# Kernel tuning notes

Measured on AMD Instinct MI355X. Metric: run time of the kernel, lower is better.

Reference implementation:

```python
import jax, jax.numpy as jnp
import numpy as np

B, N, C, H, W = 8, 512, 3, 16, 16
K, P, E = 2, 4, 1           # K: hop levels == filter taps, P: attn heads, E: edge feature sets
SLOPE = 0.2                 # LeakyReLU slope in attention
GAT_DIMS = {'d0': (128, 128), 'd1': (512, 32), 'u0': (128, 64),
            'u1': (256, 128), 's0': (128, 128), 's1': (512, 64)}


def _conv(x, w, b):
    pad = w.shape[-1] // 2
    y = jax.lax.conv_general_dilated(x, w, (1, 1), [(pad, pad), (pad, pad)],
                                     dimension_numbers=('NCHW', 'OIHW', 'NCHW'))
    return y + b[None, :, None, None]


def _gat(x, S, wk, wq, wf, b):
    # x: (B,G,N); S: (B,E,N,N) binary GSO. KeyQuery attention + K-tap attentional filter.
    key = jnp.einsum('pegf,bgn->bpefn', wk, x)
    qry = jnp.einsum('pegf,bgn->bpefn', wq, x)
    # scores[...,n,m]: logit of node n attending to neighbor m
    scores = jax.nn.leaky_relu(jnp.einsum('bpefn,bpefm->bpenm', qry, key), SLOPE)
    mask = (jnp.abs(S) > 1e-9)[:, None]                    # (B,1,E,N,N)
    aij = jnp.where(mask, jax.nn.softmax(jnp.where(mask, scores, -1e9), axis=-1), 0.0)
    Pn, En, Kt, G, F = wf.shape
    xk = jnp.broadcast_to(x[:, None, None], (x.shape[0], Pn, En, G, x.shape[-1]))
    zs = [xk]
    for _ in range(Kt - 1):
        xk = jnp.einsum('bpegm,bpenm->bpegn', xk, aij)     # attention-weighted diffusion
        zs.append(xk)
    z = jnp.stack(zs, axis=3)                              # (B,P,E,K,G,N)
    y = jnp.einsum('bpekgn,pekgf->bpfn', z, wf) + b[None, None, :, None]
    y = jax.nn.relu(y)                                     # nonlinearity before head concat
    return y.reshape(y.shape[0], Pn * F, y.shape[-1])      # (B, P*F, N)


def _forward(x, Slist, conv0_w, conv0_b, conv1_w, conv1_b, flat_w, flat_b,
             d0_wk, d0_wq, d0_wf, d0_b, d1_wk, d1_wq, d1_wf, d1_b,
             u0_wk, u0_wq, u0_wf, u0_b, u1_wk, u1_wq, u1_wf, u1_b,
             s0_wk, s0_wq, s0_wf, s0_b, s1_wk, s1_wq, s1_wf, s1_b,
             dec0_w, dec0_b, dec1_w, dec1_b):
    Bn, Nn = x.shape[0], x.shape[1]
    h = x.reshape(Bn * Nn, C, H, W)
    e = jax.nn.relu(_conv(h, conv0_w, conv0_b))
    e = jax.nn.relu(_conv(e, conv1_w, conv1_b))
    e = e + h                                              # RES connection after encoder
    f = jax.nn.relu(e.reshape(Bn * Nn, -1) @ flat_w.T + flat_b)
    g = f.reshape(Bn, -1, Nn)                              # faithful torch reshape to (B, F, N)
    S0, S1 = Slist[:, 0:1], Slist[:, 1:2]
    p0 = g
    p1 = _gat(p0, S0, d0_wk, d0_wq, d0_wf, d0_b)           # downward pass
    p2 = _gat(p1, S1, d1_wk, d1_wq, d1_wf, d1_b)
    # upward pass + shortcuts (upward[l] uses S[K-l-1]; shortcut[K-1-l] on p[K-1-l])
    u0 = _gat(p2, S1, u0_wk, u0_wq, u0_wf, u0_b) + _gat(p1, S1, s1_wk, s1_wq, s1_wf, s1_b)
    u1 = _gat(u0, S0, u1_wk, u1_wq, u1_wf, u1_b) + _gat(p0, S0, s0_wk, s0_wq, s0_wf, s0_b)
    d = jax.nn.relu(u1.reshape(Bn * Nn, -1) @ dec0_w.T + dec0_b)
    out = jax.nn.softmax(d @ dec1_w.T + dec1_b, axis=-1)   # nn.Softmax() -> dim=1 on 2D input
    return out.reshape(Bn, Nn, -1)


def setup_inputs() -> dict:
    key = jax.random.key(0)
    ks = iter(jax.random.split(key, 64))
    def nrm(shape, s=0.1):
        return jax.random.normal(next(ks), shape, jnp.float32) * s
    x = jax.random.normal(next(ks), (B, N, C, H, W), jnp.float32)
    adj = (jax.random.uniform(next(ks), (B, K, N, N)) < 0.02).astype(jnp.float32)
    Slist = jnp.clip(adj + jnp.eye(N, dtype=jnp.float32)[None, None], 0.0, 1.0)
    inp = {'x': x, 'Slist': Slist,
           'conv0_w': nrm((32, C, 3, 3)), 'conv0_b': nrm((32,)),
           'conv1_w': nrm((C, 32, 3, 3)), 'conv1_b': nrm((C,)),
           'flat_w': nrm((128, C * H * W)), 'flat_b': nrm((128,))}
    for pre, (G, F) in GAT_DIMS.items():
        inp[pre + '_wk'] = nrm((P, E, G, F))
        inp[pre + '_wq'] = nrm((P, E, G, F))
        inp[pre + '_wf'] = nrm((P, E, K, G, F))
        inp[pre + '_b'] = nrm((F,))
    inp.update({'dec0_w': nrm((256, 512)), 'dec0_b': nrm((256,)),
                'dec1_w': nrm((5, 256)), 'dec1_b': nrm((5,))})
    return inp


def reference(x, Slist, conv0_w, conv0_b, conv1_w, conv1_b, flat_w, flat_b,
              d0_wk, d0_wq, d0_wf, d0_b, d1_wk, d1_wq, d1_wf, d1_b,
              u0_wk, u0_wq, u0_wf, u0_b, u1_wk, u1_wq, u1_wf, u1_b,
              s0_wk, s0_wq, s0_wf, s0_b, s1_wk, s1_wq, s1_wf, s1_b,
              dec0_w, dec0_b, dec1_w, dec1_b):
    return _forward(x, Slist, conv0_w, conv0_b, conv1_w, conv1_b, flat_w, flat_b,
                    d0_wk, d0_wq, d0_wf, d0_b, d1_wk, d1_wq, d1_wf, d1_b,
                    u0_wk, u0_wq, u0_wf, u0_b, u1_wk, u1_wq, u1_wf, u1_b,
                    s0_wk, s0_wq, s0_wf, s0_b, s1_wk, s1_wq, s1_wf, s1_b,
                    dec0_w, dec0_b, dec1_w, dec1_b)
```

## Files before the change

kernel.cpp:

```cpp
#include <hip/hip_runtime.h>
#include <hip/hip_bf16.h>
#include <math.h>

typedef unsigned short u16;
typedef unsigned int   u32;
typedef unsigned long long u64;

#define CAP 48

__device__ __forceinline__ float tof(u16 u){
  union { u32 i; float f; } v; v.i = ((u32)u) << 16; return v.f;
}
__device__ __forceinline__ u16 fromf(float f){
  union { float f; u32 i; } v; v.f = f;
  u32 x = v.i;
  return (u16)((x + 0x7fffu + ((x >> 16) & 1u)) >> 16);
}

__global__ void detect_dtype(const void* xp, int* flag){
  if(threadIdx.x == 0 && blockIdx.x == 0){
    const u16* p = (const u16*)xp;
    int outl = 0;
    for(int i = 0; i < 128; i++){
      u16 u = p[2*i];
      int e = (u >> 7) & 0xFF;
      if(u != 0 && (e < 100 || e > 140)) outl++;
    }
    *flag = (outl > 32) ? 1 : 0;
  }
}

struct WArgs {
  const void* p[34];
  int sz[34];
  int off[35];
};

__global__ __launch_bounds__(256) void convert_weights(WArgs wa, const int* flag,
                                                       float* __restrict__ arena, int total){
  int i = blockIdx.x * 256 + threadIdx.x;
  if(i >= total) return;
  int isf = *flag;
  int t = 0;
  while(wa.off[t+1] <= i) t++;
  int j = i - wa.off[t];
  float v = 0.f;
  if(j < wa.sz[t])
    v = isf ? ((const float*)wa.p[t])[j] : tof(((const u16*)wa.p[t])[j]);
  arena[i] = v;
}

__global__ __launch_bounds__(256) void transpose_w(const float* __restrict__ src,
                                                   float* __restrict__ dst, int R, int C){
  int i = blockIdx.x * 256 + threadIdx.x;
  if(i < R*C){
    int r = i / C, c = i - r*C;
    dst[(size_t)c*R + r] = src[i];
  }
}

__global__ __launch_bounds__(64) void build_nbr(const void* __restrict__ S,
                                                int* __restrict__ nbr_idx,
                                                int* __restrict__ nbr_cnt,
                                                const int* __restrict__ flag){
  int isf = *flag;
  int row  = blockIdx.x;
  int lane = threadIdx.x;
  int cnt = 0;
  for(int c = 0; c < 8; c++){
    int m = c*64 + lane;
    size_t idx = (size_t)row * 512 + m;
    float sv = isf ? ((const float*)S)[idx] : tof(((const u16*)S)[idx]);
    bool pred = fabsf(sv) > 1e-9f;
    unsigned long long mask = __ballot(pred);
    int pos = cnt + __popcll(mask & ((1ull << lane) - 1ull));
    if(pred && pos < CAP) nbr_idx[(size_t)row*CAP + pos] = m;
    cnt += __popcll(mask);
  }
  if(lane == 0) nbr_cnt[row] = cnt > CAP ? CAP : cnt;
}

__global__ __launch_bounds__(256) void encoder_conv(
    const void* __restrict__ x, const int* __restrict__ flag,
    const float* __restrict__ w0, const float* __restrict__ b0,
    const float* __restrict__ w1, const float* __restrict__ b1,
    float* __restrict__ e1n)
{
  __shared__ float xpad[3][18][18];
  __shared__ float e0p[16][18][18];

  int isf = *flag;
  int tid = threadIdx.x;
  size_t img = blockIdx.x;
  int py = tid >> 4, px = tid & 15;

  float* z1 = &xpad[0][0][0];
  for(int i = tid; i < 972; i += 256) z1[i] = 0.f;
  float* z2 = &e0p[0][0][0];
  for(int i = tid; i < 5184; i += 256) z2[i] = 0.f;
  __syncthreads();

  #pragma unroll
  for(int i = 0; i < 3; i++){
    size_t gi = img*768 + i*256 + tid;
    xpad[i][1+py][1+px] = isf ? ((const float*)x)[gi] : tof(((const u16*)x)[gi]);
  }
  __syncthreads();

  float acc1[3] = {0.f, 0.f, 0.f};

  for(int grp = 0; grp < 2; grp++){
    float acc0[16];
    #pragma unroll
    for(int o = 0; o < 16; o++) acc0[o] = 0.f;
    for(int i = 0; i < 3; i++){
      float rr[9];
      #pragma unroll
      for(int ky = 0; ky < 3; ky++)
        #pragma unroll
        for(int kx = 0; kx < 3; kx++)
          rr[ky*3+kx] = xpad[i][py+ky][px+kx];
      #pragma unroll
      for(int o = 0; o < 16; o++){
        #pragma unroll
        for(int t = 0; t < 9; t++)
          acc0[o] = fmaf(rr[t], w0[(grp*16+o)*27 + i*9 + t], acc0[o]);
      }
    }
    __syncthreads();
    #pragma unroll
    for(int o = 0; o < 16; o++)
      e0p[o][1+py][1+px] = fmaxf(acc0[o] + b0[grp*16 + o], 0.f);
    __syncthreads();

    for(int i = 0; i < 16; i++){
      float rr[9];
      #pragma unroll
      for(int ky = 0; ky < 3; ky++)
        #pragma unroll
        for(int kx = 0; kx < 3; kx++)
          rr[ky*3+kx] = e0p[i][py+ky][px+kx];
      int ic = grp*16 + i;
      #pragma unroll
      for(int o = 0; o < 3; o++){
        #pragma unroll
        for(int t = 0; t < 9; t++)
          acc1[o] = fmaf(rr[t], w1[o*288 + ic*9 + t], acc1[o]);
      }
    }
  }

  #pragma unroll
  for(int o = 0; o < 3; o++)
    e1n[img*768 + o*256 + tid] = fmaxf(acc1[o] + b1[o], 0.f) + xpad[o][1+py][1+px];
}

__global__ __launch_bounds__(256) void gemm_flat(
    const float* __restrict__ e1n, const float* __restrict__ fwT,
    const float* __restrict__ fb, float* __restrict__ g)
{
  __shared__ float As[16][68];
  __shared__ float Bs[16][68];
  int tid = threadIdx.x;
  int n0 = blockIdx.x * 64, m0 = blockIdx.y * 64;

  int lk = tid >> 4;
  int l4 = (tid & 15) * 4;
  int br = tid >> 2;
  int bc = (tid & 3) * 4;

  float acc[4][4];
  #pragma unroll
  for(int i = 0; i < 4; i++)
    #pragma unroll
    for(int jj = 0; jj < 4; jj++) acc[i][jj] = 0.f;

  int tm = tid >> 4, tn = tid & 15;
  for(int kt = 0; kt < 48; kt++){
    int k0 = kt*16;
    *(float4*)&As[lk][l4] = *(const float4*)&fwT[(size_t)(k0 + lk)*128 + m0 + l4];
    float4 bv = *(const float4*)&e1n[(size_t)(n0 + br)*768 + k0 + bc];
    Bs[bc+0][br] = bv.x; Bs[bc+1][br] = bv.y; Bs[bc+2][br] = bv.z; Bs[bc+3][br] = bv.w;
    __syncthreads();
    #pragma unroll
    for(int kk = 0; kk < 16; kk++){
      float4 a  = *(const float4*)&As[kk][tm*4];
      float4 xx = *(const float4*)&Bs[kk][tn*4];
      float av[4]  = {a.x, a.y, a.z, a.w};
      float xvv[4] = {xx.x, xx.y, xx.z, xx.w};
      #pragma unroll
      for(int i = 0; i < 4; i++)
        #pragma unroll
        for(int jj = 0; jj < 4; jj++)
          acc[i][jj] = fmaf(av[i], xvv[jj], acc[i][jj]);
    }
    __syncthreads();
  }

  #pragma unroll
  for(int jj = 0; jj < 4; jj++){
    int img = n0 + tn*4 + jj;
    float4 r = make_float4(fmaxf(acc[0][jj] + fb[m0+tm*4+0], 0.f),
                           fmaxf(acc[1][jj] + fb[m0+tm*4+1], 0.f),
                           fmaxf(acc[2][jj] + fb[m0+tm*4+2], 0.f),
                           fmaxf(acc[3][jj] + fb[m0+tm*4+3], 0.f));
    *(float4*)&g[(size_t)img*128 + m0 + tm*4] = r;
  }
}

struct KqP { const float* X; const float* wk; const float* wq; float* kqT;
             int G, F, my; };

__global__ __launch_bounds__(256) void gemm_kq2(KqP A, KqP B)
{
  __shared__ float Ws[32*68];
  __shared__ float Xs[32*68];
  int tid = threadIdx.x;
  int by = blockIdx.y;
  KqP P = (by < A.my) ? A : B;
  int lby = (by < A.my) ? by : (by - A.my);
  int bp = blockIdx.z;
  int b = bp >> 2, p = bp & 3;
  int n0 = blockIdx.x * 64, m0 = lby * 64;
  const float* Xb = P.X + (size_t)b * P.G * 512;

  int lk = tid >> 4;
  int l4 = (tid & 15) * 4;

  int mg = m0 + l4;
  int quad = mg / P.F;
  int mq = mg - quad * P.F;
  size_t GF = (size_t)P.G * P.F;
  const float* wb = (quad == 0 ? P.wk : P.wq) + (size_t)p * GF + mq;

  float acc[4][4];
  #pragma unroll
  for(int i = 0; i < 4; i++)
    #pragma unroll
    for(int jj = 0; jj < 4; jj++) acc[i][jj] = 0.f;

  int tm = tid >> 4, tn = tid & 15;
  int KT = P.G / 32;
  for(int kt = 0; kt < KT; kt++){
    int k = kt*32 + lk;
    *(float4*)&Ws[lk*68 + l4]      = *(const float4*)(wb + (size_t)k * P.F);
    *(float4*)&Ws[(lk+16)*68 + l4] = *(const float4*)(wb + (size_t)(k+16) * P.F);
    *(float4*)&Xs[lk*68 + l4]      = *(const float4*)(Xb + (size_t)k * 512 + n0 + l4);
    *(float4*)&Xs[(lk+16)*68 + l4] = *(const float4*)(Xb + (size_t)(k+16) * 512 + n0 + l4);
    __syncthreads();
    #pragma unroll
    for(int kk = 0; kk < 32; kk++){
      float4 a  = *(const float4*)&Ws[kk*68 + tm*4];
      float4 xx = *(const float4*)&Xs[kk*68 + tn*4];
      float av[4]  = {a.x, a.y, a.z, a.w};
      float xvv[4] = {xx.x, xx.y, xx.z, xx.w};
      #pragma unroll
      for(int i = 0; i < 4; i++)
        #pragma unroll
        for(int jj = 0; jj < 4; jj++)
          acc[i][jj] = fmaf(av[i], xvv[jj], acc[i][jj]);
    }
    __syncthreads();
  }

  int F2 = 2*P.F;
  float* ob = P.kqT + (size_t)bp * 512 * F2;
  #pragma unroll
  for(int jj = 0; jj < 4; jj++){
    float* orow = ob + (size_t)(n0 + tn*4 + jj) * F2 + m0 + tm*4;
    #pragma unroll
    for(int i = 0; i < 4; i++) orow[i] = acc[i][jj];
  }
}

__global__ __launch_bounds__(256) void gemm_kqK64(
    const float* __restrict__ X,
    const float* __restrict__ wk, const float* __restrict__ wq,
    float* __restrict__ kqT, int G, int F)
{
  __shared__ float Ws[64][68];
  __shared__ float Xs[64][68];
  int tid = threadIdx.x;
  int bp = blockIdx.z;
  int b = bp >> 2, p = bp & 3;
  int n0 = blockIdx.x * 64, m0 = blockIdx.y * 64;
  const float* Xb = X + (size_t)b * G * 512;

  int lk = tid >> 4;
  int l4 = (tid & 15) * 4;

  int mg = m0 + l4;
  int quad = mg / F;
  int mq = mg - quad * F;
  size_t GF = (size_t)G * F;
  const float* wb = (quad == 0 ? wk : wq) + (size_t)p * GF + mq;

  float acc[4][4];
  #pragma unroll
  for(int i = 0; i < 4; i++)
    #pragma unroll
    for(int jj = 0; jj < 4; jj++) acc[i][jj] = 0.f;

  int tm = tid >> 4, tn = tid & 15;
  int KT = G / 64;
  for(int kt = 0; kt < KT; kt++){
    #pragma unroll
    for(int kb = 0; kb < 4; kb++){
      int k = kt*64 + lk + kb*16;
      *(float4*)&Ws[lk + kb*16][l4] = *(const float4*)(wb + (size_t)k * F);
      *(float4*)&Xs[lk + kb*16][l4] = *(const float4*)(Xb + (size_t)k * 512 + n0 + l4);
    }
    __syncthreads();
    #pragma unroll
    for(int kk = 0; kk < 64; kk++){
      float4 a  = *(const float4*)&Ws[kk][tm*4];
      float4 xx = *(const float4*)&Xs[kk][tn*4];
      float av[4]  = {a.x, a.y, a.z, a.w};
      float xvv[4] = {xx.x, xx.y, xx.z, xx.w};
      #pragma unroll
      for(int i = 0; i < 4; i++)
        #pragma unroll
        for(int jj = 0; jj < 4; jj++)
          acc[i][jj] = fmaf(av[i], xvv[jj], acc[i][jj]);
    }
    __syncthreads();
  }

  int F2 = 2*F;
  float* ob = kqT + (size_t)bp * 512 * F2;
  #pragma unroll
  for(int jj = 0; jj < 4; jj++){
    float* orow = ob + (size_t)(n0 + tn*4 + jj) * F2 + m0 + tm*4;
    #pragma unroll
    for(int i = 0; i < 4; i++) orow[i] = acc[i][jj];
  }
}

struct AtP { const float* kqT; u64* ctrl; int F, s; };

__global__ __launch_bounds__(256) void attn2(
    AtP A, AtP B,
    const int* __restrict__ nbr_idx, const int* __restrict__ nbr_cnt)
{
  __shared__ float qs[16][132];
  __shared__ float sc[16][CAP];
  __shared__ float red[16][2];
  int tid = threadIdx.x;
  int n0 = blockIdx.x * 16;
  int bp = blockIdx.y;
  AtP P = (blockIdx.z == 0) ? A : B;
  int b = bp >> 2;
  int F = P.F;
  int F2 = 2*F;
  const float* kqT = P.kqT;

  int F4 = F >> 2;
  for(int i = tid; i < 16*F4; i += 256){
    int r = i / F4, c4 = (i - r*F4) * 4;
    *(float4*)&qs[r][c4] =
      *(const float4*)&kqT[((size_t)bp*512 + n0 + r)*F2 + F + c4];
  }
  __syncthreads();

  int r = tid >> 4;
  int t = tid & 15;
  int n = n0 + r;
  int srow = (b*2 + P.s)*512 + n;
  int cnt = nbr_cnt[srow];
  const int* il = nbr_idx + (size_t)srow * CAP;

  for(int j = t; j < cnt; j += 16){
    int m = il[j];
    const float* krow = kqT + ((size_t)bp*512 + m)*F2;
    float a = 0.f;
    for(int f = 0; f < F; f += 4){
      float4 k4 = *(const float4*)&krow[f];
      a = fmaf(qs[r][f],   k4.x, a);
      a = fmaf(qs[r][f+1], k4.y, a);
      a = fmaf(qs[r][f+2], k4.z, a);
      a = fmaf(qs[r][f+3], k4.w, a);
    }
    sc[r][j] = a >= 0.f ? a : 0.2f * a;
  }
  __syncthreads();

  if(t == 0){
    float mx = -1e30f;
    for(int j = 0; j < cnt; j++) mx = fmaxf(mx, sc[r][j]);
    float ssum = 0.f;
    for(int j = 0; j < cnt; j++) ssum += expf(sc[r][j] - mx);
    red[r][0] = mx; red[r][1] = ssum;
  }
  __syncthreads();

  float mx = red[r][0], ssum = red[r][1];
  u64* crow = P.ctrl + ((size_t)bp*512 + n)*CAP;
  for(int j = t; j < cnt; j += 16){
    float w = expf(sc[r][j] - mx) / ssum;
    crow[j] = (u64)__float_as_uint(w) | ((u64)(u32)il[j] << 32);
  }
}

struct FiP { const float* X; const u64* ctrl; float* Xp; int G, s, gy; };

__global__ __launch_bounds__(256) void fill_Xp4(
    FiP A, FiP B, const int* __restrict__ nbr_cnt)
{
  __shared__ float xi[512*18];

  int tid = threadIdx.x;
  int by = blockIdx.y;
  FiP P = (by < A.gy) ? A : B;
  int lby = (by < A.gy) ? by : (by - A.gy);
  int n0 = blockIdx.x * 64;
  int g0 = lby * 16;
  int bp = blockIdx.z;
  int b = bp >> 2;
  int srow0 = (b*2 + P.s)*512 + n0;

  const float* Xb = P.X + ((size_t)b * P.G + g0) * 512;
  for(int i = tid; i < 16*512; i += 256){
    int gl = i >> 9, m = i & 511;
    xi[m*18 + gl] = Xb[(size_t)gl*512 + m];
  }

  int n_l = tid & 63;
  int q   = tid >> 6;
  int cnt = nbr_cnt[srow0 + n_l];
  const u64* cn = P.ctrl + ((size_t)bp*512 + n0 + n_l)*CAP;
  __syncthreads();

  const float* xq = &xi[4*q];
  float a0=0.f, a1=0.f, a2=0.f, a3=0.f;
  for(int j0 = 0; j0 < cnt; j0 += 4){
    u64 c0 = cn[j0], c1 = cn[j0+1], c2 = cn[j0+2], c3 = cn[j0+3];
    int m0 = (int)(c0 >> 32) & 511;
    int m1 = (int)(c1 >> 32) & 511;
    int m2 = (int)(c2 >> 32) & 511;
    int m3 = (int)(c3 >> 32) & 511;
    float w0 = __uint_as_float((u32)c0);
    float w1 = (j0+1 < cnt) ? __uint_as_float((u32)c1) : 0.f;
    float w2 = (j0+2 < cnt) ? __uint_as_float((u32)c2) : 0.f;
    float w3 = (j0+3 < cnt) ? __uint_as_float((u32)c3) : 0.f;
    float2 g0a = *(const float2*)&xq[m0*18], g0b = *(const float2*)&xq[m0*18 + 2];
    float2 g1a = *(const float2*)&xq[m1*18], g1b = *(const float2*)&xq[m1*18 + 2];
    float2 g2a = *(const float2*)&xq[m2*18], g2b = *(const float2*)&xq[m2*18 + 2];
    float2 g3a = *(const float2*)&xq[m3*18], g3b = *(const float2*)&xq[m3*18 + 2];
    a0 = fmaf(w0, g0a.x, a0); a1 = fmaf(w0, g0a.y, a1);
    a2 = fmaf(w0, g0b.x, a2); a3 = fmaf(w0, g0b.y, a3);
    a0 = fmaf(w1, g1a.x, a0); a1 = fmaf(w1, g1a.y, a1);
    a2 = fmaf(w1, g1b.x, a2); a3 = fmaf(w1, g1b.y, a3);
    a0 = fmaf(w2, g2a.x, a0); a1 = fmaf(w2, g2a.y, a1);
    a2 = fmaf(w2, g2b.x, a2); a3 = fmaf(w2, g2b.y, a3);
    a0 = fmaf(w3, g3a.x, a0); a1 = fmaf(w3, g3a.y, a1);
    a2 = fmaf(w3, g3b.x, a2); a3 = fmaf(w3, g3b.y, a3);
  }

  float* ob = P.Xp + ((size_t)bp * P.G + g0 + 4*q) * 512 + n0 + n_l;
  ob[0]    = a0;
  ob[512]  = a1;
  ob[1024] = a2;
  ob[1536] = a3;
}

struct YP { const float* X; const float* Xp; const float* wf; const float* bias;
            float* out; int G, F, PF, acc, my; };

__global__ __launch_bounds__(256) void gemm_y2_32(YP A, YP B)
{
  __shared__ float Ws[32*68];
  __shared__ float Xs[32*68];
  int tid = threadIdx.x;
  int by = blockIdx.y;
  YP P = (by < A.my) ? A : B;
  int lby = (by < A.my) ? by : (by - A.my);
  int bp = blockIdx.z;
  int b = bp >> 2, p = bp & 3;
  int n0 = blockIdx.x * 64, m0 = lby * 64;
  int G = P.G, F = P.F;

  int lk = tid >> 4;
  int l4 = (tid & 15) * 4;
  int mg = m0 + l4;
  int fcl = mg < F ? mg : (F - 4);
  size_t GF2 = (size_t)2 * G * F;
  const float* wb = P.wf + (size_t)p * GF2 + fcl;

  float acc[4][4];
  #pragma unroll
  for(int i = 0; i < 4; i++)
    #pragma unroll
    for(int jj = 0; jj < 4; jj++) acc[i][jj] = 0.f;

  int tm = tid >> 4, tn = tid & 15;
  int KT = (2*G) / 32;
  for(int kt = 0; kt < KT; kt++){
    int c0 = kt*32 + lk;
    int c1 = c0 + 16;
    const float* xr0 = (c0 < G) ? (P.X  + ((size_t)b  * G + c0      ) * 512)
                                : (P.Xp + ((size_t)bp * G + (c0 - G)) * 512);
    const float* xr1 = (c1 < G) ? (P.X  + ((size_t)b  * G + c1      ) * 512)
                                : (P.Xp + ((size_t)bp * G + (c1 - G)) * 512);
    *(float4*)&Ws[lk*68 + l4]      = *(const float4*)(wb + (size_t)c0 * F);
    *(float4*)&Ws[(lk+16)*68 + l4] = *(const float4*)(wb + (size_t)c1 * F);
    *(float4*)&Xs[lk*68 + l4]      = *(const float4*)(xr0 + n0 + l4);
    *(float4*)&Xs[(lk+16)*68 + l4] = *(const float4*)(xr1 + n0 + l4);
    __syncthreads();
    #pragma unroll
    for(int kk = 0; kk < 32; kk++){
      float4 a  = *(const float4*)&Ws[kk*68 + tm*4];
      float4 xx = *(const float4*)&Xs[kk*68 + tn*4];
      float av[4]  = {a.x, a.y, a.z, a.w};
      float xvv[4] = {xx.x, xx.y, xx.z, xx.w};
      #pragma unroll
      for(int i = 0; i < 4; i++)
        #pragma unroll
        for(int jj = 0; jj < 4; jj++)
          acc[i][jj] = fmaf(av[i], xvv[jj], acc[i][jj]);
    }
    __syncthreads();
  }

  int mrow = m0 + tm*4;
  if(mrow < F){
    float* ob = P.out + ((size_t)b * P.PF + (size_t)p * F + mrow) * 512 + n0 + tn*4;
    #pragma unroll
    for(int i = 0; i < 4; i++){
      float bv = P.bias[mrow + i];
      float4 r = make_float4(fmaxf(acc[i][0] + bv, 0.f),
                             fmaxf(acc[i][1] + bv, 0.f),
                             fmaxf(acc[i][2] + bv, 0.f),
                             fmaxf(acc[i][3] + bv, 0.f));
      float* dst = ob + (size_t)i * 512;
      if(P.acc){
        float4 old = *(float4*)dst;
        r.x += old.x; r.y += old.y; r.z += old.z; r.w += old.w;
      }
      *(float4*)dst = r;
    }
  }
}

__global__ __launch_bounds__(256) void gemm_y2_K64(YP A, YP B)
{
  __shared__ float Ws[64*68];
  __shared__ float Xs[64*68];
  int tid = threadIdx.x;
  int by = blockIdx.y;
  YP P = (by < A.my) ? A : B;
  int lby = (by < A.my) ? by : (by - A.my);
  int bp = blockIdx.z;
  int b = bp >> 2, p = bp & 3;
  int n0 = blockIdx.x * 64, m0 = lby * 64;
  int G = P.G, F = P.F;

  int lk = tid >> 4;
  int l4 = (tid & 15) * 4;
  int mg = m0 + l4;
  int fcl = mg < F ? mg : (F - 4);
  size_t GF2 = (size_t)2 * G * F;
  const float* wb = P.wf + (size_t)p * GF2 + fcl;

  float acc[4][4];
  #pragma unroll
  for(int i = 0; i < 4; i++)
    #pragma unroll
    for(int jj = 0; jj < 4; jj++) acc[i][jj] = 0.f;

  int tm = tid >> 4, tn = tid & 15;
  int KT = (2*G) / 64;
  for(int kt = 0; kt < KT; kt++){
    #pragma unroll
    for(int kb = 0; kb < 4; kb++){
      int c = kt*64 + lk + kb*16;
      const float* xr = (c < G) ? (P.X  + ((size_t)b  * G + c      ) * 512)
                                : (P.Xp + ((size_t)bp * G + (c - G)) * 512);
      *(float4*)&Ws[(lk + kb*16)*68 + l4] = *(const float4*)(wb + (size_t)c * F);
      *(float4*)&Xs[(lk + kb*16)*68 + l4] = *(const float4*)(xr + n0 + l4);
    }
    __syncthreads();
    #pragma unroll
    for(int kk = 0; kk < 64; kk++){
      float4 a  = *(const float4*)&Ws[kk*68 + tm*4];
      float4 xx = *(const float4*)&Xs[kk*68 + tn*4];
      float av[4]  = {a.x, a.y, a.z, a.w};
      float xvv[4] = {xx.x, xx.y, xx.z, xx.w};
      #pragma unroll
      for(int i = 0; i < 4; i++)
        #pragma unroll
        for(int jj = 0; jj < 4; jj++)
          acc[i][jj] = fmaf(av[i], xvv[jj], acc[i][jj]);
    }
    __syncthreads();
  }

  int mrow = m0 + tm*4;
  if(mrow < F){
    float* ob = P.out + ((size_t)b * P.PF + (size_t)p * F + mrow) * 512 + n0 + tn*4;
    #pragma unroll
    for(int i = 0; i < 4; i++){
      float bv = P.bias[mrow + i];
      float4 r = make_float4(fmaxf(acc[i][0] + bv, 0.f),
                             fmaxf(acc[i][1] + bv, 0.f),
                             fmaxf(acc[i][2] + bv, 0.f),
                             fmaxf(acc[i][3] + bv, 0.f));
      float* dst = ob + (size_t)i * 512;
      if(P.acc){
        float4 old = *(float4*)dst;
        r.x += old.x; r.y += old.y; r.z += old.z; r.w += old.w;
      }
      *(float4*)dst = r;
    }
  }
}

__global__ __launch_bounds__(256) void add_vec(float* __restrict__ dst,
                                               const float* __restrict__ src, int n4){
  int i = blockIdx.x * 256 + threadIdx.x;
  if(i < n4){
    float4 a = ((const float4*)dst)[i];
    float4 b = ((const float4*)src)[i];
    a.x += b.x; a.y += b.y; a.z += b.z; a.w += b.w;
    ((float4*)dst)[i] = a;
  }
}

__global__ __launch_bounds__(256) void gemm_dec0(
    const float* __restrict__ u1, const float* __restrict__ w0T,
    const float* __restrict__ b0, float* __restrict__ d)
{
  __shared__ float As[16][68];
  __shared__ float Bs[16][68];
  int tid = threadIdx.x;
  int n0 = blockIdx.x * 64;
  int m0 = blockIdx.y * 64;

  int lk = tid >> 4;
  int l4 = (tid & 15) * 4;
  int br = tid >> 2;
  int bc = (tid & 3) * 4;

  float acc[4][4];
  #pragma unroll
  for(int i = 0; i < 4; i++)
    #pragma unroll
    for(int jj = 0; jj < 4; jj++) acc[i][jj] = 0.f;

  int tm = tid >> 4, tn = tid & 15;
  for(int kt = 0; kt < 32; kt++){
    int k0 = kt*16;
    *(float4*)&As[lk][l4] = *(const float4*)&w0T[(size_t)(k0 + lk)*256 + m0 + l4];
    float4 bv = *(const float4*)&u1[(size_t)(n0 + br)*512 + k0 + bc];
    Bs[bc+0][br] = bv.x; Bs[bc+1][br] = bv.y; Bs[bc+2][br] = bv.z; Bs[bc+3][br] = bv.w;
    __syncthreads();
    #pragma unroll
    for(int kk = 0; kk < 16; kk++){
      float4 a  = *(const float4*)&As[kk][tm*4];
      float4 xx = *(const float4*)&Bs[kk][tn*4];
      float av[4]  = {a.x, a.y, a.z, a.w};
      float xvv[4] = {xx.x, xx.y, xx.z, xx.w};
      #pragma unroll
      for(int i = 0; i < 4; i++)
        #pragma unroll
        for(int jj = 0; jj < 4; jj++)
          acc[i][jj] = fmaf(av[i], xvv[jj], acc[i][jj]);
    }
    __syncthreads();
  }

  #pragma unroll
  for(int jj = 0; jj < 4; jj++){
    int row = n0 + tn*4 + jj;
    float4 r = make_float4(fmaxf(acc[0][jj] + b0[m0+tm*4+0], 0.f),
                           fmaxf(acc[1][jj] + b0[m0+tm*4+1], 0.f),
                           fmaxf(acc[2][jj] + b0[m0+tm*4+2], 0.f),
                           fmaxf(acc[3][jj] + b0[m0+tm*4+3], 0.f));
    *(float4*)&d[(size_t)row*256 + m0 + tm*4] = r;
  }
}

__global__ __launch_bounds__(64) void decoder2(
    const float* __restrict__ d,
    const float* __restrict__ w1, const float* __restrict__ b1,
    const int* __restrict__ flag, void* __restrict__ outp)
{
  __shared__ float ds[256];
  __shared__ float lg[5];
  int r = blockIdx.x, lane = threadIdx.x;
  for(int i = lane; i < 256; i += 64) ds[i] = d[(size_t)r*256 + i];
  __syncthreads();

  if(lane < 5){
    float a = 0.f;
    const float* wr = w1 + (size_t)lane * 256;
    for(int i = 0; i < 256; i++) a = fmaf(ds[i], wr[i], a);
    lg[lane] = a + b1[lane];
  }
  __syncthreads();
  if(lane < 5){
    float mx = lg[0];
    for(int i = 1; i < 5; i++) mx = fmaxf(mx, lg[i]);
    float ssum = 0.f;
    for(int i = 0; i < 5; i++) ssum += expf(lg[i] - mx);
    float v = expf(lg[lane] - mx) / ssum;
    if(*flag) ((float*)outp)[(size_t)r*5 + lane] = v;
    else      ((u16*)outp)[(size_t)r*5 + lane] = fromf(v);
  }
}

extern "C" void kernel_launch(void* const* d_in, const int* in_sizes, int n_in,
                              void* d_out, int out_size, void* d_ws, size_t ws_size,
                              hipStream_t stream)
{
  (void)n_in; (void)out_size; (void)ws_size;
  const void* x = d_in[0];
  const void* S = d_in[1];

  float* wsf   = (float*)d_ws;
  int*   flag  = (int*)d_ws;
  float* arena = wsf + 1024;

  WArgs wa;
  long long aoff[35]; aoff[0] = 0;
  for(int t = 0; t < 34; t++){
    wa.p[t]  = d_in[2 + t];
    wa.sz[t] = in_sizes[2 + t];
    wa.off[t] = (int)aoff[t];
    aoff[t+1] = aoff[t] + ((in_sizes[2 + t] + 15) & ~15);
  }
  wa.off[34] = (int)aoff[34];
  int total = (int)aoff[34];

  size_t cur = 1024 + (size_t)((total + 1023) & ~1023);
  float* g    = wsf + cur; cur += 524288;
  float* p1   = wsf + cur; cur += 2097152;
  float* p2   = wsf + cur; cur += 524288;
  float* u0b  = wsf + cur; cur += 1048576;
  float* u0c  = wsf + cur; cur += 1048576;
  float* u1c  = wsf + cur; cur += 2097152;
  float* u1b  = p1;
  u64*   ctrlA= (u64*)(wsf + cur); cur += (size_t)32*512*CAP*2;
  u64*   ctrlB= (u64*)(wsf + cur); cur += (size_t)32*512*CAP*2;
  float* fwT  = wsf + cur; cur += 98304;
  float* dw0T = wsf + cur; cur += 131072;
  int*   ncnt = (int*)(wsf + cur); cur += 8192;
  int*   nidx = (int*)(wsf + cur); cur += (size_t)8192 * CAP;
  float* pool = wsf + cur; cur += 10485760;

  float* e1n   = pool;
  float* kqT0  = pool;
  float* Xp0   = pool;
  float* kqT1  = pool;
  float* Xp1   = pool;
  float* kqT2  = pool;
  float* kqT3  = pool + 2097152;
  float* Xp2   = pool;
  float* Xp3   = pool + 2097152;
  float* kqT4  = pool;
  float* kqT5  = pool + 4194304;
  float* Xp4   = pool;
  float* Xp5   = pool + 4194304;
  float* dbuf  = pool;

  const float* A[34];
  for(int t = 0; t < 34; t++) A[t] = arena + aoff[t];
  const float* c0w = A[0], *c0b = A[1], *c1w = A[2], *c1b = A[3];
  const float* fw  = A[4], *fb  = A[5];
  const float *wk_[6], *wq_[6], *wf_[6], *bias_[6];
  for(int l = 0; l < 6; l++){
    wk_[l]   = A[6 + 4*l];
    wq_[l]   = A[7 + 4*l];
    wf_[l]   = A[8 + 4*l];
    bias_[l] = A[9 + 4*l];
  }
  const float* dw0 = A[30], *db0 = A[31], *dw1 = A[32], *db1 = A[33];

  detect_dtype<<<1, 64, 0, stream>>>(x, flag);
  convert_weights<<<(total + 255)/256, 256, 0, stream>>>(wa, flag, arena, total);
  transpose_w<<<(98304 + 255)/256, 256, 0, stream>>>(fw, fwT, 128, 768);
  transpose_w<<<(131072 + 255)/256, 256, 0, stream>>>(dw0, dw0T, 256, 512);
  build_nbr<<<8192, 64, 0, stream>>>(S, nidx, ncnt, flag);
  encoder_conv<<<4096, 256, 0, stream>>>(x, flag, c0w, c0b, c1w, c1b, e1n);
  gemm_flat<<<dim3(64, 2), 256, 0, stream>>>(e1n, fwT, fb, g);

  {
    KqP k0 = { g, wk_[0], wq_[0], kqT0, 128, 128, 4 };
    gemm_kq2<<<dim3(8, 4, 32), 256, 0, stream>>>(k0, k0);
    AtP a0 = { kqT0, ctrlA, 128, 0 };
    attn2<<<dim3(32, 32, 1), 256, 0, stream>>>(a0, a0, nidx, ncnt);
    FiP f0 = { g, ctrlA, Xp0, 128, 0, 8 };
    fill_Xp4<<<dim3(8, 8, 32), 256, 0, stream>>>(f0, f0, ncnt);
    YP y0 = { g, Xp0, wf_[0], bias_[0], p1, 128, 128, 512, 0, 2 };
    gemm_y2_32<<<dim3(8, 2, 32), 256, 0, stream>>>(y0, y0);
  }

  {
    gemm_kqK64<<<dim3(8, 1, 32), 256, 0, stream>>>(p1, wk_[1], wq_[1], kqT1, 512, 32);
    AtP a1 = { kqT1, ctrlA, 32, 1 };
    attn2<<<dim3(32, 32, 1), 256, 0, stream>>>(a1, a1, nidx, ncnt);
    FiP f1 = { p1, ctrlA, Xp1, 512, 1, 32 };
    fill_Xp4<<<dim3(8, 32, 32), 256, 0, stream>>>(f1, f1, ncnt);
    YP y1 = { p1, Xp1, wf_[1], bias_[1], p2, 512, 32, 128, 0, 1 };
    gemm_y2_K64<<<dim3(8, 1, 32), 256, 0, stream>>>(y1, y1);
  }

  {
    KqP k2 = { p2, wk_[2], wq_[2], kqT2, 128, 64, 2 };
    KqP k3 = { p1, wk_[5], wq_[5], kqT3, 512, 64, 2 };
    gemm_kq2<<<dim3(8, 4, 32), 256, 0, stream>>>(k2, k3);
    AtP a2 = { kqT2, ctrlA, 64, 1 };
    AtP a3 = { kqT3, ctrlB, 64, 1 };
    attn2<<<dim3(32, 32, 2), 256, 0, stream>>>(a2, a3, nidx, ncnt);
    FiP f2 = { p2, ctrlA, Xp2, 128, 1, 8 };
    FiP f3 = { p1, ctrlB, Xp3, 512, 1, 32 };
    fill_Xp4<<<dim3(8, 40, 32), 256, 0, stream>>>(f2, f3, ncnt);
    YP y2 = { p2, Xp2, wf_[2], bias_[2], u0b, 128, 64, 256, 0, 1 };
    YP y3 = { p1, Xp3, wf_[5], bias_[5], u0c, 512, 64, 256, 0, 1 };
    gemm_y2_K64<<<dim3(8, 2, 32), 256, 0, stream>>>(y2, y3);
    add_vec<<<1024, 256, 0, stream>>>(u0b, u0c, 262144);
  }

  {
    KqP k4 = { u0b, wk_[3], wq_[3], kqT4, 256, 128, 4 };
    KqP k5 = { g,   wk_[4], wq_[4], kqT5, 128, 128, 4 };
    gemm_kq2<<<dim3(8, 8, 32), 256, 0, stream>>>(k4, k5);
    AtP a4 = { kqT4, ctrlA, 128, 0 };
    AtP a5 = { kqT5, ctrlB, 128, 0 };
    attn2<<<dim3(32, 32, 2), 256, 0, stream>>>(a4, a5, nidx, ncnt);
    FiP f4 = { u0b, ctrlA, Xp4, 256, 0, 16 };
    FiP f5 = { g,   ctrlB, Xp5, 128, 0, 8 };
    fill_Xp4<<<dim3(8, 24, 32), 256, 0, stream>>>(f4, f5, ncnt);
    YP y4 = { u0b, Xp4, wf_[3], bias_[3], u1b, 256, 128, 512, 0, 2 };
    YP y5 = { g,   Xp5, wf_[4], bias_[4], u1c, 128, 128, 512, 0, 2 };
    gemm_y2_32<<<dim3(8, 4, 32), 256, 0, stream>>>(y4, y5);
    add_vec<<<2048, 256, 0, stream>>>(u1b, u1c, 524288);
  }

  gemm_dec0<<<dim3(64, 4), 256, 0, stream>>>(u1b, dw0T, db0, dbuf);
  decoder2<<<4096, 64, 0, stream>>>(dbuf, dw1, db1, flag, d_out);
}
```

Measured before the change: 917.3 us.

## Move independent s0 GAT layer into the d1 stage batched launches

The s0 layer, which depends only on the encoder output g, is moved from the last GAT stage into the d1 stage. Its key/query GEMM, attention, fill and output GEMM now share launches with d1 through the dual-parameter kernels. The separate K64 key/query kernel is removed and d1 goes through the generic gemm_kq2 path instead. The goal is to fill the GPU better during the small d1 stage, at the cost of more pool memory and a different kernel for d1.

```diff
diff --git a/kernel.cpp b/kernel.cpp
--- a/kernel.cpp
+++ b/kernel.cpp
@@ -265,69 +265,6 @@
 
   int F2 = 2*P.F;
   float* ob = P.kqT + (size_t)bp * 512 * F2;
-  #pragma unroll
-  for(int jj = 0; jj < 4; jj++){
-    float* orow = ob + (size_t)(n0 + tn*4 + jj) * F2 + m0 + tm*4;
-    #pragma unroll
-    for(int i = 0; i < 4; i++) orow[i] = acc[i][jj];
-  }
-}
-
-__global__ __launch_bounds__(256) void gemm_kqK64(
-    const float* __restrict__ X,
-    const float* __restrict__ wk, const float* __restrict__ wq,
-    float* __restrict__ kqT, int G, int F)
-{
-  __shared__ float Ws[64][68];
-  __shared__ float Xs[64][68];
-  int tid = threadIdx.x;
-  int bp = blockIdx.z;
-  int b = bp >> 2, p = bp & 3;
-  int n0 = blockIdx.x * 64, m0 = blockIdx.y * 64;
-  const float* Xb = X + (size_t)b * G * 512;
-
-  int lk = tid >> 4;
-  int l4 = (tid & 15) * 4;
-
-  int mg = m0 + l4;
-  int quad = mg / F;
-  int mq = mg - quad * F;
-  size_t GF = (size_t)G * F;
-  const float* wb = (quad == 0 ? wk : wq) + (size_t)p * GF + mq;
-
-  float acc[4][4];
-  #pragma unroll
-  for(int i = 0; i < 4; i++)
-    #pragma unroll
-    for(int jj = 0; jj < 4; jj++) acc[i][jj] = 0.f;
-
-  int tm = tid >> 4, tn = tid & 15;
-  int KT = G / 64;
-  for(int kt = 0; kt < KT; kt++){
-    #pragma unroll
-    for(int kb = 0; kb < 4; kb++){
-      int k = kt*64 + lk + kb*16;
-      *(float4*)&Ws[lk + kb*16][l4] = *(const float4*)(wb + (size_t)k * F);
-      *(float4*)&Xs[lk + kb*16][l4] = *(const float4*)(Xb + (size_t)k * 512 + n0 + l4);
-    }
-    __syncthreads();
-    #pragma unroll
-    for(int kk = 0; kk < 64; kk++){
-      float4 a  = *(const float4*)&Ws[kk][tm*4];
-      float4 xx = *(const float4*)&Xs[kk][tn*4];
-      float av[4]  = {a.x, a.y, a.z, a.w};
-      float xvv[4] = {xx.x, xx.y, xx.z, xx.w};
-      #pragma unroll
-      for(int i = 0; i < 4; i++)
-        #pragma unroll
-        for(int jj = 0; jj < 4; jj++)
-          acc[i][jj] = fmaf(av[i], xvv[jj], acc[i][jj]);
-    }
-    __syncthreads();
-  }
-
-  int F2 = 2*F;
-  float* ob = kqT + (size_t)bp * 512 * F2;
   #pragma unroll
   for(int jj = 0; jj < 4; jj++){
     float* orow = ob + (size_t)(n0 + tn*4 + jj) * F2 + m0 + tm*4;
@@ -751,15 +688,15 @@
   float* kqT0  = pool;
   float* Xp0   = pool;
   float* kqT1  = pool;
+  float* kqT5  = pool + 4194304;
   float* Xp1   = pool;
+  float* Xp5   = pool + 8388608;
   float* kqT2  = pool;
   float* kqT3  = pool + 2097152;
   float* Xp2   = pool;
   float* Xp3   = pool + 2097152;
   float* kqT4  = pool;
-  float* kqT5  = pool + 4194304;
   float* Xp4   = pool;
-  float* Xp5   = pool + 4194304;
   float* dbuf  = pool;
 
   const float* A[34];
@@ -795,13 +732,18 @@
   }
 
   {
-    gemm_kqK64<<<dim3(8, 1, 32), 256, 0, stream>>>(p1, wk_[1], wq_[1], kqT1, 512, 32);
-    AtP a1 = { kqT1, ctrlA, 32, 1 };
-    attn2<<<dim3(32, 32, 1), 256, 0, stream>>>(a1, a1, nidx, ncnt);
+    KqP k1 = { p1, wk_[1], wq_[1], kqT1, 512,  32, 1 };
+    KqP k5 = { g,  wk_[4], wq_[4], kqT5, 128, 128, 4 };
+    gemm_kq2<<<dim3(8, 5, 32), 256, 0, stream>>>(k1, k5);
+    AtP a1 = { kqT1, ctrlA,  32, 1 };
+    AtP a5 = { kqT5, ctrlB, 128, 0 };
+    attn2<<<dim3(32, 32, 2), 256, 0, stream>>>(a1, a5, nidx, ncnt);
     FiP f1 = { p1, ctrlA, Xp1, 512, 1, 32 };
-    fill_Xp4<<<dim3(8, 32, 32), 256, 0, stream>>>(f1, f1, ncnt);
-    YP y1 = { p1, Xp1, wf_[1], bias_[1], p2, 512, 32, 128, 0, 1 };
-    gemm_y2_K64<<<dim3(8, 1, 32), 256, 0, stream>>>(y1, y1);
+    FiP f5 = { g,  ctrlB, Xp5, 128, 0, 8 };
+    fill_Xp4<<<dim3(8, 40, 32), 256, 0, stream>>>(f1, f5, ncnt);
+    YP y1 = { p1, Xp1, wf_[1], bias_[1], p2,  512,  32, 128, 0, 1 };
+    YP y5 = { g,  Xp5, wf_[4], bias_[4], u1c, 128, 128, 512, 0, 2 };
+    gemm_y2_K64<<<dim3(8, 3, 32), 256, 0, stream>>>(y1, y5);
   }
 
   {
@@ -822,17 +764,13 @@
 
   {
     KqP k4 = { u0b, wk_[3], wq_[3], kqT4, 256, 128, 4 };
-    KqP k5 = { g,   wk_[4], wq_[4], kqT5, 128, 128, 4 };
-    gemm_kq2<<<dim3(8, 8, 32), 256, 0, stream>>>(k4, k5);
+    gemm_kq2<<<dim3(8, 4, 32), 256, 0, stream>>>(k4, k4);
     AtP a4 = { kqT4, ctrlA, 128, 0 };
-    AtP a5 = { kqT5, ctrlB, 128, 0 };
-    attn2<<<dim3(32, 32, 2), 256, 0, stream>>>(a4, a5, nidx, ncnt);
+    attn2<<<dim3(32, 32, 1), 256, 0, stream>>>(a4, a4, nidx, ncnt);
     FiP f4 = { u0b, ctrlA, Xp4, 256, 0, 16 };
-    FiP f5 = { g,   ctrlB, Xp5, 128, 0, 8 };
-    fill_Xp4<<<dim3(8, 24, 32), 256, 0, stream>>>(f4, f5, ncnt);
+    fill_Xp4<<<dim3(8, 16, 32), 256, 0, stream>>>(f4, f4, ncnt);
     YP y4 = { u0b, Xp4, wf_[3], bias_[3], u1b, 256, 128, 512, 0, 2 };
-    YP y5 = { g,   Xp5, wf_[4], bias_[4], u1c, 128, 128, 512, 0, 2 };
-    gemm_y2_32<<<dim3(8, 4, 32), 256, 0, stream>>>(y4, y5);
+    gemm_y2_32<<<dim3(8, 2, 32), 256, 0, stream>>>(y4, y4);
     add_vec<<<2048, 256, 0, stream>>>(u1b, u1c, 524288);
   }
 
```

Result: faster. 875.5 us (-4.6%).
